# Optimization experiments

Hardware: AMD Instinct MI355X
Metric: run time of the kernel (lower is better)

Reference implementation:

```python
import jax, jax.numpy as jnp
import numpy as np

D_MODEL = 1024
NUM_HEADS = 16
HEAD_DIM = D_MODEL // NUM_HEADS
THETA = 10000.0
BATCH = 2
SEQ = 2048


def _apply_rope(x, positions):
    # x: (b, h, s, hd), positions: (b, s) int
    hd = x.shape[-1]
    inv_freq = 1.0 / (THETA ** (jnp.arange(0, hd, 2, dtype=jnp.float32) / hd))  # (hd/2,)
    ang = positions.astype(jnp.float32)[:, None, :, None] * inv_freq  # (b,1,s,hd/2)
    cos, sin = jnp.cos(ang), jnp.sin(ang)
    x1 = x[..., 0::2]
    x2 = x[..., 1::2]
    r1 = x1 * cos - x2 * sin
    r2 = x1 * sin + x2 * cos
    return jnp.stack([r1, r2], axis=-1).reshape(x.shape)


def setup_inputs() -> dict:
    key = jax.random.key(0)
    ks = jax.random.split(key, 5)
    scale = 1.0 / np.sqrt(D_MODEL)
    x = jax.random.normal(ks[0], (BATCH, SEQ, D_MODEL), dtype=jnp.float32)
    token_positions = jnp.broadcast_to(jnp.arange(SEQ, dtype=jnp.int32), (BATCH, SEQ))
    W_q = jax.random.normal(ks[1], (D_MODEL, D_MODEL), dtype=jnp.float32) * scale
    W_k = jax.random.normal(ks[2], (D_MODEL, D_MODEL), dtype=jnp.float32) * scale
    W_v = jax.random.normal(ks[3], (D_MODEL, D_MODEL), dtype=jnp.float32) * scale
    W_o = jax.random.normal(ks[4], (D_MODEL, D_MODEL), dtype=jnp.float32) * scale
    return {"x": x, "token_positions": token_positions, "W_q": W_q, "W_k": W_k, "W_v": W_v, "W_o": W_o}


def reference(x, token_positions, W_q, W_k, W_v, W_o):
    b, s, _ = x.shape
    h, hd = NUM_HEADS, HEAD_DIM
    # bias-free Linear: y = x @ W^T, W: (out, in)
    def proj(W):
        return jnp.einsum('bsd,ed->bse', x, W).reshape(b, s, h, hd).transpose(0, 2, 1, 3)
    Q = _apply_rope(proj(W_q), token_positions)
    K = _apply_rope(proj(W_k), token_positions)
    V = proj(W_v)
    scores = jnp.einsum('bhqd,bhkd->bhqk', Q, K) / jnp.sqrt(jnp.float32(hd))
    causal = jnp.triu(jnp.full((s, s), -jnp.inf, dtype=scores.dtype), k=1)
    attn = jax.nn.softmax(scores + causal, axis=-1)
    Z = jnp.einsum('bhqk,bhkd->bhqd', attn, V)
    Z = Z.transpose(0, 2, 1, 3).reshape(b, s, h * hd)
    return jnp.einsum('bse,de->bsd', Z, W_o)
```

## Files before the change

### kernel.cpp

```cpp
#include <hip/hip_runtime.h>
#include <hip/hip_bf16.h>


#define BATCH 2
#define SEQ   2048
#define NH    16
#define HD    64
#define DM    1024
#define MTOT  (BATCH*SEQ)

typedef __attribute__((ext_vector_type(8))) short bf16x8;
typedef __attribute__((ext_vector_type(4))) float f32x4;
typedef __attribute__((ext_vector_type(4))) unsigned int u32x4;
typedef unsigned short u16;
typedef unsigned int   u32;

__device__ __forceinline__ float b2f(u16 h){ return __uint_as_float(((u32)h) << 16); }
__device__ __forceinline__ u16 f2b(float f){
  u32 u = __float_as_uint(f);
  u32 r = (u + 0x7FFFu + ((u >> 16) & 1u)) >> 16;
  return (u16)r;
}
__device__ __forceinline__ u16 cvt1(float f){
  __hip_bfloat16 h = __float2bfloat16(f);
  return *reinterpret_cast<u16*>(&h);
}
__device__ __forceinline__ u32 pk2(float lo, float hi){
  return (u32)cvt1(lo) | ((u32)cvt1(hi) << 16);
}
__device__ __forceinline__ f32x4 mfma16(bf16x8 a, bf16x8 b, f32x4 c){
  return __builtin_amdgcn_mfma_f32_16x16x32_bf16(a, b, c, 0, 0, 0);
}
__device__ __forceinline__ void gload_lds16(const u16* g, u16* l){
  __builtin_amdgcn_global_load_lds((const __attribute__((address_space(1))) unsigned int*)g,
                                   (__attribute__((address_space(3))) unsigned int*)l, 16, 0, 0);
}

__global__ __launch_bounds__(256) void cvt_all(const float* __restrict__ x,
    const float* __restrict__ wq, const float* __restrict__ wk,
    const float* __restrict__ wv, const float* __restrict__ wo,
    u16* __restrict__ xb, u16* __restrict__ wb)
{
  const long NX = (long)MTOT * DM;
  const long NW = (long)DM * DM;
  const long tot4 = (NX + 4*NW) >> 2;
  for (long t = (long)blockIdx.x*blockDim.x + threadIdx.x; t < tot4;
       t += (long)gridDim.x*blockDim.x){
    long e = t << 2;
    const float* s; u16* d;
    if (e < NX){ s = x + e; d = xb + e; }
    else {
      long j = e - NX; int z = (int)(j >> 20);
      const float* ws = (z==0)?wq:(z==1)?wk:(z==2)?wv:wo;
      s = ws + (j & (NW-1)); d = wb + j;
    }
    float4 v = *(const float4*)s;
    u32 lo = (u32)f2b(v.x) | ((u32)f2b(v.y) << 16);
    u32 hi = (u32)f2b(v.z) | ((u32)f2b(v.w) << 16);
    uint2 o; o.x = lo; o.y = hi;
    *(uint2*)d = o;
  }
}

__global__ __launch_bounds__(256) void rope_table(float2* __restrict__ tab){
  int t = blockIdx.x*blockDim.x + threadIdx.x;
  if (t >= SEQ*32) return;
  int s = t >> 5, i = t & 31;
  float inv = 1.0f / powf(10000.0f, (float)i * (1.0f/32.0f));
  float a = (float)s * inv;
  tab[t] = make_float2(cosf(a), sinf(a));
}

__global__ __launch_bounds__(256) void gemm_qkv(const u16* __restrict__ xb,
                                                const u16* __restrict__ wb,
                                                u16* __restrict__ Qd, u16* __restrict__ Kd,
                                                u16* __restrict__ Vt,
                                                const float2* __restrict__ tab,
                                                const int* __restrict__ pos)
{
  __shared__ u16 Alds[128*64];
  __shared__ u16 Blds[64*64];
  const int fid = blockIdx.x;
  const int xj = fid & 7, tt = fid >> 3;
  const int mb = (tt/48)*8 + xj;
  const int rest = tt % 48;
  const int nb = rest & 15, z = rest >> 4;
  const u16* Bm = wb + (long)z * DM * DM;
  const int nbase = nb*64, mbase = mb*128;
  const int tid = threadIdx.x;
  const int w = tid >> 6, l = tid & 63, g = l >> 4, c = l & 15;
  const int wr = (w >> 1)*64, wc = (w & 1)*32;
  const int srow = l >> 3;
  const int scol = ((l & 7) ^ srow)*8;
  const u16* Ag = xb + (long)(mbase + w*32 + srow)*DM + scol;
  const u16* Bg = Bm + (long)(nbase + w*16 + srow)*DM + scol;
  u16* Alb = Alds + w*2048;
  u16* Blb = Blds + w*1024;
  f32x4 acc[4][2] = {};

  for (int k0 = 0; k0 < DM; k0 += 64){
    __syncthreads();
    #pragma unroll
    for (int i = 0; i < 4; i++)
      gload_lds16(Ag + k0 + (long)(8*i)*DM, Alb + i*512);
    #pragma unroll
    for (int i = 0; i < 2; i++)
      gload_lds16(Bg + k0 + (long)(8*i)*DM, Blb + i*512);
    __syncthreads();
    #pragma unroll
    for (int ks = 0; ks < 2; ks++){
      bf16x8 af[4], bfr[2];
      #pragma unroll
      for (int mi = 0; mi < 4; mi++){
        int row = wr + mi*16 + c;
        af[mi] = *(const bf16x8*)&Alds[row*64 + (((ks*4 + g) ^ (row & 7))*8)];
      }
      #pragma unroll
      for (int nj = 0; nj < 2; nj++){
        int row = wc + nj*16 + c;
        bfr[nj] = *(const bf16x8*)&Blds[row*64 + (((ks*4 + g) ^ (row & 7))*8)];
      }
      #pragma unroll
      for (int mi = 0; mi < 4; mi++)
        #pragma unroll
        for (int nj = 0; nj < 2; nj++)
          acc[mi][nj] = mfma16(af[mi], bfr[nj], acc[mi][nj]);
    }
  }

  if (z == 2){
    #pragma unroll
    for (int mi = 0; mi < 4; mi++){
      int row0 = mbase + wr + mi*16 + 4*g;
      int bb = row0 >> 11, s0 = row0 & (SEQ-1);
      #pragma unroll
      for (int nj = 0; nj < 2; nj++){
        int col = nbase + wc + nj*16 + c;
        int hh = col >> 6, d = col & 63;
        ushort4 v;
        v.x = cvt1(acc[mi][nj][0]); v.y = cvt1(acc[mi][nj][1]);
        v.z = cvt1(acc[mi][nj][2]); v.w = cvt1(acc[mi][nj][3]);
        *(ushort4*)&Vt[((long)(bb*NH + hh)*HD + d)*SEQ + s0] = v;
      }
    }
  } else {
    u16* Out = (z == 0) ? Qd : Kd;
    const float scale = (z == 0) ? 0.125f*1.44269504089f : 1.f;
    const bool even = (c & 1) == 0;
    #pragma unroll
    for (int mi = 0; mi < 4; mi++){
      #pragma unroll
      for (int r = 0; r < 4; r++){
        int row = mbase + wr + mi*16 + 4*g + r;
        int bb = row >> 11, s = row & (SEQ-1);
        int p = pos[bb*SEQ + s];
        if (p < 0) p = 0; if (p >= SEQ) p = SEQ - 1;
        #pragma unroll
        for (int nj = 0; nj < 2; nj++){
          int col = nbase + wc + nj*16 + c;
          float2 cs = tab[p*32 + ((col & 63) >> 1)];
          float own = acc[mi][nj][r];
          float prt = __shfl_xor(own, 1);
          float rr = even ? (own*cs.x - prt*cs.y) : (prt*cs.y + own*cs.x);
          rr *= scale;
          Out[(long)row*DM + col] = cvt1(rr);
        }
      }
    }
  }
}

__global__ __launch_bounds__(256) void gemm_out(const u16* __restrict__ Zb,
                                                const u16* __restrict__ wob,
                                                float* __restrict__ out)
{
  __shared__ u16 Alds[128*64];
  __shared__ u16 Blds[64*64];
  const int fid = blockIdx.x;
  const int xj = fid & 7, tt = fid >> 3;
  const int mb = (tt/16)*8 + xj;
  const int nb = tt % 16;
  const int nbase = nb*64, mbase = mb*128;
  const int tid = threadIdx.x;
  const int w = tid >> 6, l = tid & 63, g = l >> 4, c = l & 15;
  const int wr = (w >> 1)*64, wc = (w & 1)*32;
  const int srow = l >> 3;
  const int scol = ((l & 7) ^ srow)*8;
  const u16* Ag = Zb  + (long)(mbase + w*32 + srow)*DM + scol;
  const u16* Bg = wob + (long)(nbase + w*16 + srow)*DM + scol;
  u16* Alb = Alds + w*2048;
  u16* Blb = Blds + w*1024;
  f32x4 acc[4][2] = {};

  for (int k0 = 0; k0 < DM; k0 += 64){
    __syncthreads();
    #pragma unroll
    for (int i = 0; i < 4; i++)
      gload_lds16(Ag + k0 + (long)(8*i)*DM, Alb + i*512);
    #pragma unroll
    for (int i = 0; i < 2; i++)
      gload_lds16(Bg + k0 + (long)(8*i)*DM, Blb + i*512);
    __syncthreads();
    #pragma unroll
    for (int ks = 0; ks < 2; ks++){
      bf16x8 af[4], bfr[2];
      #pragma unroll
      for (int mi = 0; mi < 4; mi++){
        int row = wr + mi*16 + c;
        af[mi] = *(const bf16x8*)&Alds[row*64 + (((ks*4 + g) ^ (row & 7))*8)];
      }
      #pragma unroll
      for (int nj = 0; nj < 2; nj++){
        int row = wc + nj*16 + c;
        bfr[nj] = *(const bf16x8*)&Blds[row*64 + (((ks*4 + g) ^ (row & 7))*8)];
      }
      #pragma unroll
      for (int mi = 0; mi < 4; mi++)
        #pragma unroll
        for (int nj = 0; nj < 2; nj++)
          acc[mi][nj] = mfma16(af[mi], bfr[nj], acc[mi][nj]);
    }
  }
  #pragma unroll
  for (int mi = 0; mi < 4; mi++)
    #pragma unroll
    for (int nj = 0; nj < 2; nj++)
      #pragma unroll
      for (int r = 0; r < 4; r++){
        int row = mbase + wr + mi*16 + 4*g + r;
        int col = nbase + wc + nj*16 + c;
        out[(long)row*DM + col] = acc[mi][nj][r];
      }
}

__device__ __forceinline__ int kinv(int s){
  return (s & 32) | ((s & 16) >> 2) | ((s & 12) << 1) | (s & 3);
}

__global__ __launch_bounds__(256) void attn(const u16* __restrict__ Q, const u16* __restrict__ K,
                                            const u16* __restrict__ Vt,
                                            u16* __restrict__ Opart, float* __restrict__ Lsum)
{
  const int fid = blockIdx.x;
  const int xj = fid & 7, tt = fid >> 3;
  const int grp = (tt >> 5)*8 + xj;
  const int within = tt & 31;
  const int h = grp & 15, b = grp >> 4;
  const int pair = within >> 1;
  const int half = within & 1;
  const int tid = threadIdx.x, w = tid >> 6, l = tid & 63, g = l >> 4, c = l & 15;
  const u16* Kp = K  + (long)(b*SEQ)*DM + h*HD;
  const u16* Vp = Vt + (long)(b*NH + h)*HD*SEQ;

  __shared__ u16 KV[2][2][64][64];
  u16* kv = &KV[0][0][0][0];

  const int lrow0 = w*8 + (l >> 3), lrow1 = lrow0 + 32, lch = l & 7;
  const long ks0 = (long)kinv(lrow0)*DM + ((lch ^ (lrow0 & 7))*8);
  const long ks1 = (long)kinv(lrow1)*DM + ((lch ^ (lrow1 & 7))*8);
  const long vs0 = (long)lrow0*SEQ + ((lch ^ (lrow0 & 7))*8);
  const long vs1 = (long)lrow1*SEQ + ((lch ^ (lrow1 & 7))*8);
  const int kd0 = w*512, kd1 = kd0 + 2048;
  const int vd0 = 4096 + kd0, vd1 = 4096 + kd1;

  const int cswz = c & 7;
  const int ra0 = c*64 + (((0 + g) ^ cswz)*8);
  const int ra1 = c*64 + (((4 + g) ^ cswz)*8);

  bf16x8 ones;
  #pragma unroll
  for (int j = 0; j < 8; j++) ones[j] = (short)0x3F80;

  int bufo = 0;
  #pragma unroll 1
  for (int seg = 0; seg < 2; ++seg){
    const int qt = seg ? (31 - pair) : pair;
    const int qbase = qt*64;
    const int qrow = qbase + w*16;
    const u16* Qp = Q + (long)(b*SEQ + qrow)*DM + h*HD;
    bf16x8 qf0 = *(const bf16x8*)(Qp + c*DM + g*8);
    bf16x8 qf1 = *(const bf16x8*)(Qp + c*DM + 32 + g*8);

    const int ntH0  = (qt + 2) >> 1;
    const int tstart = half ? ntH0 : 0;
    const int tend   = half ? (qt + 1) : ntH0;

    f32x4 accz[4] = {};
    f32x4 lacc = {};

    if (tstart < tend){
      __syncthreads();
      const u16* kgp = Kp + (long)(tstart*64)*DM;
      const u16* vgp = Vp + tstart*64;
      gload_lds16(kgp + ks0, kv + bufo + kd0);
      gload_lds16(kgp + ks1, kv + bufo + kd1);
      gload_lds16(vgp + vs0, kv + bufo + vd0);
      gload_lds16(vgp + vs1, kv + bufo + vd1);
      kgp += (long)64*DM; vgp += 64;

      for (int t = tstart; t < tend; ++t){
        const int kbase = t*64;
        __syncthreads();

        if (t < tend-1){
          int nbo = bufo ^ 8192;
          gload_lds16(kgp + ks0, kv + nbo + kd0);
          gload_lds16(kgp + ks1, kv + nbo + kd1);
          gload_lds16(vgp + vs0, kv + nbo + vd0);
          gload_lds16(vgp + vs1, kv + nbo + vd1);
          kgp += (long)64*DM; vgp += 64;
        }

        const u16* kvb = kv + bufo;

        f32x4 s[4];
        __builtin_amdgcn_s_setprio(1);
        #pragma unroll
        for (int sub = 0; sub < 4; sub++){
          bf16x8 ka0 = *(const bf16x8*)(kvb + ra0 + sub*1024);
          bf16x8 ka1 = *(const bf16x8*)(kvb + ra1 + sub*1024);
          f32x4 z4 = {};
          z4 = mfma16(ka0, qf0, z4);
          z4 = mfma16(ka1, qf1, z4);
          s[sub] = z4;
        }
        __builtin_amdgcn_s_setprio(0);

        const bool edge = (kbase + 63 > qrow);
        const int q = qrow + c;
        if (edge){
          #pragma unroll
          for (int sub = 0; sub < 4; sub++)
            #pragma unroll
            for (int r = 0; r < 4; r++){
              int key = kbase + ((sub >> 1) << 5) + 8*g + ((sub & 1) << 2) + r;
              if (key > q) s[sub][r] = -1e30f;
            }
        }
        #pragma unroll
        for (int sub = 0; sub < 4; sub++)
          #pragma unroll
          for (int r = 0; r < 4; r++)
            s[sub][r] = exp2f(s[sub][r]);

        u32x4 p0, p1;
        p0[0] = pk2(s[0][0], s[0][1]); p0[1] = pk2(s[0][2], s[0][3]);
        p0[2] = pk2(s[1][0], s[1][1]); p0[3] = pk2(s[1][2], s[1][3]);
        p1[0] = pk2(s[2][0], s[2][1]); p1[1] = pk2(s[2][2], s[2][3]);
        p1[2] = pk2(s[3][0], s[3][1]); p1[3] = pk2(s[3][2], s[3][3]);
        bf16x8 pf0 = __builtin_bit_cast(bf16x8, p0);
        bf16x8 pf1 = __builtin_bit_cast(bf16x8, p1);

        __builtin_amdgcn_s_setprio(1);
        lacc = mfma16(pf0, ones, lacc);
        lacc = mfma16(pf1, ones, lacc);
        #pragma unroll
        for (int dt = 0; dt < 4; dt++){
          bf16x8 vf0 = *(const bf16x8*)(kvb + 4096 + ra0 + dt*1024);
          bf16x8 vf1 = *(const bf16x8*)(kvb + 4096 + ra1 + dt*1024);
          accz[dt] = mfma16(pf0, vf0, accz[dt]);
          accz[dt] = mfma16(pf1, vf1, accz[dt]);
        }
        __builtin_amdgcn_s_setprio(0);

        if (t < tend-1) bufo ^= 8192;
      }
    }

    const int pbase = (((b*NH + h)*32 + qt)*2 + half);
    if (c == 0){
      #pragma unroll
      for (int r = 0; r < 4; r++)
        Lsum[pbase*64 + w*16 + 4*g + r] = lacc[r];
    }
    u16* Op = Opart + (long)pbase*(64*64);
    #pragma unroll
    for (int dt = 0; dt < 4; dt++)
      #pragma unroll
      for (int r = 0; r < 4; r++)
        Op[(w*16 + 4*g + r)*64 + dt*16 + c] = cvt1(accz[dt][r]);
  }
}

__global__ __launch_bounds__(256) void attn_combine(const u16* __restrict__ Opart,
                                                    const float* __restrict__ Lsum,
                                                    u16* __restrict__ Z)
{
  const int qt = blockIdx.x, h = blockIdx.y, b = blockIdx.z;
  const int p0 = ((b*NH + h)*32 + qt)*2, p1 = p0 + 1;
  const int row = threadIdx.x >> 2;
  const int d0  = (threadIdx.x & 3)*16;
  float inv = 1.f / (Lsum[p0*64 + row] + Lsum[p1*64 + row]);
  const u16* o0 = Opart + ((long)p0*64 + row)*64 + d0;
  const u16* o1 = Opart + ((long)p1*64 + row)*64 + d0;
  const int s = qt*64 + row;
  u16* zp = Z + (long)(b*SEQ + s)*DM + h*HD + d0;
  #pragma unroll
  for (int j = 0; j < 2; j++){
    bf16x8 va = *(const bf16x8*)(o0 + j*8);
    bf16x8 vb = *(const bf16x8*)(o1 + j*8);
    bf16x8 ov;
    #pragma unroll
    for (int e = 0; e < 8; e++){
      float z = (b2f((u16)va[e]) + b2f((u16)vb[e]))*inv;
      ov[e] = (short)cvt1(z);
    }
    *(bf16x8*)(zp + j*8) = ov;
  }
}

extern "C" void kernel_launch(void* const* d_in, const int* in_sizes, int n_in,
                              void* d_out, int out_size, void* d_ws, size_t ws_size,
                              hipStream_t stream)
{
  const float* x  = (const float*)d_in[0];
  const int*   pos= (const int*)d_in[1];
  const float* wq = (const float*)d_in[2];
  const float* wk = (const float*)d_in[3];
  const float* wv = (const float*)d_in[4];
  const float* wo = (const float*)d_in[5];
  float* out = (float*)d_out;

  const long NX = (long)MTOT*DM;
  const long NW = (long)DM*DM;
  char* p = (char*)d_ws;
  u16* xb   = (u16*)p;  p += NX*2;
  u16* wb   = (u16*)p;  p += 4*NW*2;
  u16* Qd   = (u16*)p;  p += NX*2;
  u16* Kd   = (u16*)p;  p += NX*2;
  u16* Vt   = (u16*)p;  p += NX*2;
  u16* Zb   = (u16*)p;  p += NX*2;
  float2* tab = (float2*)p; p += (long)SEQ*32*sizeof(float2);
  u16* Opart = (u16*)p;  p += 2L*NX*2;
  float* Lsum = (float*)p; p += 2048L*64*sizeof(float);
  (void)ws_size; (void)n_in; (void)in_sizes; (void)out_size;

  hipLaunchKernelGGL(cvt_all,     dim3(2048),      dim3(256), 0, stream, x, wq, wk, wv, wo, xb, wb);
  hipLaunchKernelGGL(rope_table,  dim3(256),       dim3(256), 0, stream, tab);
  hipLaunchKernelGGL(gemm_qkv,    dim3(1536),      dim3(256), 0, stream, xb, wb, Qd, Kd, Vt, tab, pos);
  hipLaunchKernelGGL(attn,        dim3(1024),      dim3(256), 0, stream, Qd, Kd, Vt, Opart, Lsum);
  hipLaunchKernelGGL(attn_combine,dim3(32,16,2),   dim3(256), 0, stream, Opart, Lsum, Zb);
  hipLaunchKernelGGL(gemm_out,    dim3(512),       dim3(256), 0, stream, Zb, wb + 3*NW, out);
}
```

Measured before the change: 117.2 us.

## Split attention KV range into quarters and drop LDS double buffering

```diff
diff --git a/kernel.cpp b/kernel.cpp
--- a/kernel.cpp
+++ b/kernel.cpp
@@ -243,17 +243,17 @@
 {
   const int fid = blockIdx.x;
   const int xj = fid & 7, tt = fid >> 3;
-  const int grp = (tt >> 5)*8 + xj;
-  const int within = tt & 31;
+  const int grp = (tt >> 6)*8 + xj;
+  const int within = tt & 63;
   const int h = grp & 15, b = grp >> 4;
-  const int pair = within >> 1;
-  const int half = within & 1;
+  const int pair = within >> 2;
+  const int quarter = within & 3;
   const int tid = threadIdx.x, w = tid >> 6, l = tid & 63, g = l >> 4, c = l & 15;
   const u16* Kp = K  + (long)(b*SEQ)*DM + h*HD;
   const u16* Vp = Vt + (long)(b*NH + h)*HD*SEQ;
 
-  __shared__ u16 KV[2][2][64][64];
-  u16* kv = &KV[0][0][0][0];
+  __shared__ u16 KV[2][64][64];
+  u16* kv = &KV[0][0][0];
 
   const int lrow0 = w*8 + (l >> 3), lrow1 = lrow0 + 32, lch = l & 7;
   const long ks0 = (long)kinv(lrow0)*DM + ((lch ^ (lrow0 & 7))*8);
@@ -271,7 +271,6 @@
   #pragma unroll
   for (int j = 0; j < 8; j++) ones[j] = (short)0x3F80;
 
-  int bufo = 0;
   #pragma unroll 1
   for (int seg = 0; seg < 2; ++seg){
     const int qt = seg ? (31 - pair) : pair;
@@ -281,44 +280,33 @@
     bf16x8 qf0 = *(const bf16x8*)(Qp + c*DM + g*8);
     bf16x8 qf1 = *(const bf16x8*)(Qp + c*DM + 32 + g*8);
 
-    const int ntH0  = (qt + 2) >> 1;
-    const int tstart = half ? ntH0 : 0;
-    const int tend   = half ? (qt + 1) : ntH0;
+    const int nt = qt + 1;
+    const int tstart = (quarter*nt) >> 2;
+    const int tend   = ((quarter + 1)*nt) >> 2;
 
     f32x4 accz[4] = {};
     f32x4 lacc = {};
 
     if (tstart < tend){
-      __syncthreads();
       const u16* kgp = Kp + (long)(tstart*64)*DM;
       const u16* vgp = Vp + tstart*64;
-      gload_lds16(kgp + ks0, kv + bufo + kd0);
-      gload_lds16(kgp + ks1, kv + bufo + kd1);
-      gload_lds16(vgp + vs0, kv + bufo + vd0);
-      gload_lds16(vgp + vs1, kv + bufo + vd1);
-      kgp += (long)64*DM; vgp += 64;
 
       for (int t = tstart; t < tend; ++t){
         const int kbase = t*64;
         __syncthreads();
-
-        if (t < tend-1){
-          int nbo = bufo ^ 8192;
-          gload_lds16(kgp + ks0, kv + nbo + kd0);
-          gload_lds16(kgp + ks1, kv + nbo + kd1);
-          gload_lds16(vgp + vs0, kv + nbo + vd0);
-          gload_lds16(vgp + vs1, kv + nbo + vd1);
-          kgp += (long)64*DM; vgp += 64;
-        }
-
-        const u16* kvb = kv + bufo;
+        gload_lds16(kgp + ks0, kv + kd0);
+        gload_lds16(kgp + ks1, kv + kd1);
+        gload_lds16(vgp + vs0, kv + vd0);
+        gload_lds16(vgp + vs1, kv + vd1);
+        kgp += (long)64*DM; vgp += 64;
+        __syncthreads();
 
         f32x4 s[4];
         __builtin_amdgcn_s_setprio(1);
         #pragma unroll
         for (int sub = 0; sub < 4; sub++){
-          bf16x8 ka0 = *(const bf16x8*)(kvb + ra0 + sub*1024);
-          bf16x8 ka1 = *(const bf16x8*)(kvb + ra1 + sub*1024);
+          bf16x8 ka0 = *(const bf16x8*)(kv + ra0 + sub*1024);
+          bf16x8 ka1 = *(const bf16x8*)(kv + ra1 + sub*1024);
           f32x4 z4 = {};
           z4 = mfma16(ka0, qf0, z4);
           z4 = mfma16(ka1, qf1, z4);
@@ -356,18 +344,16 @@
         lacc = mfma16(pf1, ones, lacc);
         #pragma unroll
         for (int dt = 0; dt < 4; dt++){
-          bf16x8 vf0 = *(const bf16x8*)(kvb + 4096 + ra0 + dt*1024);
-          bf16x8 vf1 = *(const bf16x8*)(kvb + 4096 + ra1 + dt*1024);
+          bf16x8 vf0 = *(const bf16x8*)(kv + 4096 + ra0 + dt*1024);
+          bf16x8 vf1 = *(const bf16x8*)(kv + 4096 + ra1 + dt*1024);
           accz[dt] = mfma16(pf0, vf0, accz[dt]);
           accz[dt] = mfma16(pf1, vf1, accz[dt]);
         }
         __builtin_amdgcn_s_setprio(0);
-
-        if (t < tend-1) bufo ^= 8192;
-      }
-    }
-
-    const int pbase = (((b*NH + h)*32 + qt)*2 + half);
+      }
+    }
+
+    const int pbase = (((b*NH + h)*32 + qt)*4 + quarter);
     if (c == 0){
       #pragma unroll
       for (int r = 0; r < 4; r++)
@@ -387,24 +373,27 @@
                                                     u16* __restrict__ Z)
 {
   const int qt = blockIdx.x, h = blockIdx.y, b = blockIdx.z;
-  const int p0 = ((b*NH + h)*32 + qt)*2, p1 = p0 + 1;
+  const int p0 = ((b*NH + h)*32 + qt)*4;
   const int row = threadIdx.x >> 2;
   const int d0  = (threadIdx.x & 3)*16;
-  float inv = 1.f / (Lsum[p0*64 + row] + Lsum[p1*64 + row]);
-  const u16* o0 = Opart + ((long)p0*64 + row)*64 + d0;
-  const u16* o1 = Opart + ((long)p1*64 + row)*64 + d0;
+  float lsum = 0.f;
+  #pragma unroll
+  for (int q = 0; q < 4; q++) lsum += Lsum[(p0 + q)*64 + row];
+  float inv = 1.f / lsum;
   const int s = qt*64 + row;
   u16* zp = Z + (long)(b*SEQ + s)*DM + h*HD + d0;
   #pragma unroll
   for (int j = 0; j < 2; j++){
-    bf16x8 va = *(const bf16x8*)(o0 + j*8);
-    bf16x8 vb = *(const bf16x8*)(o1 + j*8);
+    float acc[8] = {};
+    #pragma unroll
+    for (int q = 0; q < 4; q++){
+      bf16x8 v = *(const bf16x8*)(Opart + ((long)(p0 + q)*64 + row)*64 + d0 + j*8);
+      #pragma unroll
+      for (int e = 0; e < 8; e++) acc[e] += b2f((u16)v[e]);
+    }
     bf16x8 ov;
     #pragma unroll
-    for (int e = 0; e < 8; e++){
-      float z = (b2f((u16)va[e]) + b2f((u16)vb[e]))*inv;
-      ov[e] = (short)cvt1(z);
-    }
+    for (int e = 0; e < 8; e++) ov[e] = (short)cvt1(acc[e]*inv);
     *(bf16x8*)(zp + j*8) = ov;
   }
 }
@@ -431,14 +420,14 @@
   u16* Vt   = (u16*)p;  p += NX*2;
   u16* Zb   = (u16*)p;  p += NX*2;
   float2* tab = (float2*)p; p += (long)SEQ*32*sizeof(float2);
-  u16* Opart = (u16*)p;  p += 2L*NX*2;
-  float* Lsum = (float*)p; p += 2048L*64*sizeof(float);
+  u16* Opart = (u16*)p;  p += 4L*NX*2;
+  float* Lsum = (float*)p; p += 4096L*64*sizeof(float);
   (void)ws_size; (void)n_in; (void)in_sizes; (void)out_size;
 
   hipLaunchKernelGGL(cvt_all,     dim3(2048),      dim3(256), 0, stream, x, wq, wk, wv, wo, xb, wb);
   hipLaunchKernelGGL(rope_table,  dim3(256),       dim3(256), 0, stream, tab);
   hipLaunchKernelGGL(gemm_qkv,    dim3(1536),      dim3(256), 0, stream, xb, wb, Qd, Kd, Vt, tab, pos);
-  hipLaunchKernelGGL(attn,        dim3(1024),      dim3(256), 0, stream, Qd, Kd, Vt, Opart, Lsum);
+  hipLaunchKernelGGL(attn,        dim3(2048),      dim3(256), 0, stream, Qd, Kd, Vt, Opart, Lsum);
   hipLaunchKernelGGL(attn_combine,dim3(32,16,2),   dim3(256), 0, stream, Opart, Lsum, Zb);
   hipLaunchKernelGGL(gemm_out,    dim3(512),       dim3(256), 0, stream, Zb, wb + 3*NW, out);
 }
```

Result: slower. 124.7 us (+6.4%).
